# Kernel optimization log

Hardware: AMD Instinct MI355X
Metric: run time of the kernel (lower is better)

## Reference

```python
import jax, jax.numpy as jnp
import numpy as np

N, M = 100000, 12
A, E = 128, 64
BN_EPS = 1e-5

def batchnorm(x, gamma, beta):
    # training-mode BN over leading dim, biased variance (torch default)
    mean = jnp.mean(x, axis=0)
    var = jnp.var(x, axis=0)
    return (x - mean) * jax.lax.rsqrt(var + BN_EPS) * gamma + beta

def setup_inputs() -> dict:
    key = jax.random.key(0)
    ks = jax.random.split(key, 9)
    s_in = 1.0 / np.sqrt(2 * A + E)
    s_skip = 1.0 / np.sqrt(A)
    return {
        "atom_in_fea": jax.random.normal(ks[0], (N, A), jnp.float32),
        "nbr_fea": jax.random.normal(ks[1], (N, M, E), jnp.float32),
        "nbr_fea_idx": jax.random.randint(ks[2], (N, M), 0, N),
        "W_full": jax.random.uniform(ks[3], (2 * A + E, 2 * A), jnp.float32, -s_in, s_in),
        "b_full": jax.random.uniform(ks[4], (2 * A,), jnp.float32, -s_in, s_in),
        "gamma1": jnp.ones((2 * A,), jnp.float32),
        "beta1": jnp.zeros((2 * A,), jnp.float32),
        "gamma2": jnp.ones((A,), jnp.float32),
        "beta2": jnp.zeros((A,), jnp.float32),
        "W_skip": jax.random.uniform(ks[5], (A, A), jnp.float32, -s_skip, s_skip),
        "b_skip": jax.random.uniform(ks[6], (A,), jnp.float32, -s_skip, s_skip),
    }

def reference(atom_in_fea, nbr_fea, nbr_fea_idx, W_full, b_full,
              gamma1, beta1, gamma2, beta2, W_skip, b_skip):
    atom_nbr_fea = atom_in_fea[nbr_fea_idx]                      # [N,M,A] gather
    atom_self_fea = jnp.broadcast_to(atom_in_fea[:, None, :], (N, M, A))
    total = jnp.concatenate([atom_self_fea, atom_nbr_fea, nbr_fea], axis=2)  # [N,M,2A+E]
    gated = jnp.einsum('nmf,fg->nmg', total, W_full) + b_full    # [N,M,2A]
    gated = batchnorm(gated.reshape(-1, 2 * A), gamma1, beta1).reshape(N, M, 2 * A)
    nbr_filter, nbr_core = gated[..., :A], gated[..., A:]
    nbr_sumed = jnp.sum(jax.nn.sigmoid(nbr_filter) * jax.nn.softplus(nbr_core), axis=1)  # [N,A]
    nbr_sumed = batchnorm(nbr_sumed, gamma2, beta2)
    skip_val = atom_in_fea @ W_skip + b_skip
    return jax.nn.softplus(skip_val + nbr_sumed)
```

## Files before the change

kernel.cpp:

```cpp
#include <hip/hip_runtime.h>
#include <stdint.h>

#define N_ATOM 100000
#define M_NBR 12
#define A_FEA 128
#define E_FEA 64
#define KDIM 320
#define GDIM 256
#define ROWS (N_ATOM*M_NBR)
#define BN_EPS 1e-5f

typedef unsigned short u16;
typedef unsigned int u32;
typedef __attribute__((ext_vector_type(8))) short short8;
typedef __attribute__((ext_vector_type(4))) float f32x4;

#define S_BN1SUM 0
#define S_BN1SSQ 256
#define S_S1 512
#define S_T1 768
#define S_BN2SUM 1024
#define S_BN2SSQ 1152
#define S_S2 1280
#define S_T2 1408
#define STATS_F32 1536

#define WPQ_OFF 0
#define W3_OFF 131072
#define WSK_OFF 163840
#define STATS_OFF 196608
#define P_OFF 202752
#define PQ_BYTES ((size_t)N_ATOM*256*2)
#define Q_OFF (P_OFF + PQ_BYTES)
#define GATED_OFF (Q_OFF + PQ_BYTES)
#define GATED_BYTES ((size_t)ROWS*256*2)

__device__ __forceinline__ u16 f2bf(float x) {
    union { float f; u32 u; } v; v.f = x;
    u32 r = v.u + 0x7FFFu + ((v.u >> 16) & 1u);
    return (u16)(r >> 16);
}
__device__ __forceinline__ float bf2f(u16 u) {
    union { u32 u; float f; } v; v.u = ((u32)u) << 16;
    return v.f;
}
__device__ __forceinline__ float softplus_f(float x) {
    return fmaxf(x, 0.f) + __logf(1.f + __expf(-fabsf(x)));
}
__device__ __forceinline__ float sigmoid_f(float x) {
    return 1.f / (1.f + __expf(-x));
}

__global__ void zero_stats(float* __restrict__ stats) {
    int t = threadIdx.x;
    stats[t] = 0.f;
    stats[256 + t] = 0.f;
    stats[1024 + t] = 0.f;
}

__global__ void finalize1(const float* __restrict__ g1, const float* __restrict__ b1,
                          float* __restrict__ stats) {
    int c = threadIdx.x;
    const float inv_cnt = 1.f / (float)ROWS;
    float mean = stats[S_BN1SUM + c] * inv_cnt;
    float var  = stats[S_BN1SSQ + c] * inv_cnt - mean * mean;
    float iv = rsqrtf(var + BN_EPS);
    float s = g1[c] * iv;
    stats[S_S1 + c] = s;
    stats[S_T1 + c] = fmaf(-mean, s, b1[c]);
}

__global__ void finalize2(const float* __restrict__ g2, const float* __restrict__ b2,
                          float* __restrict__ stats) {
    int c = threadIdx.x;
    const float inv_cnt = 1.f / (float)N_ATOM;
    float mean = stats[S_BN2SUM + c] * inv_cnt;
    float var  = stats[S_BN2SSQ + c] * inv_cnt - mean * mean;
    float iv = rsqrtf(var + BN_EPS);
    float s = g2[c] * iv;
    stats[S_S2 + c] = s;
    stats[S_T2 + c] = fmaf(-mean, s, b2[c]);
}


__global__ void prep_pack_fast(const float* __restrict__ Wfull,
                               const float* __restrict__ Wskip,
                               u16* __restrict__ wpq, u16* __restrict__ w3,
                               u16* __restrict__ wsk) {
    int tid = blockIdx.x * blockDim.x + threadIdx.x;
    int l = tid & 63, fr = l & 15, fq = l >> 4;
    if (tid < 8192) {
        int ct = (tid >> 6) & 31;
        int kt = tid >> 11;
        int c = ct * 16 + fr;
        int k0 = kt * 32 + fq * 8;
        u16 tmp[8];
        #pragma unroll
        for (int i = 0; i < 8; ++i) {
            int kk = k0 + i;
            float v = (c < 256) ? Wfull[kk * GDIM + c]
                                : Wfull[(128 + kk) * GDIM + (c - 256)];
            tmp[i] = f2bf(v);
        }
        uint4 pk;
        pk.x = (u32)tmp[0] | ((u32)tmp[1] << 16);
        pk.y = (u32)tmp[2] | ((u32)tmp[3] << 16);
        pk.z = (u32)tmp[4] | ((u32)tmp[5] << 16);
        pk.w = (u32)tmp[6] | ((u32)tmp[7] << 16);
        *reinterpret_cast<uint4*>(&wpq[tid * 8]) = pk;
    } else if (tid < 10240) {
        int t2 = tid - 8192;
        int ct = (t2 >> 6) & 15;
        int kt = t2 >> 10;
        int c = ct * 16 + fr;
        int k0 = kt * 32 + fq * 8;
        u16 tmp[8];
        #pragma unroll
        for (int i = 0; i < 8; ++i) tmp[i] = f2bf(Wfull[(256 + k0 + i) * GDIM + c]);
        uint4 pk;
        pk.x = (u32)tmp[0] | ((u32)tmp[1] << 16);
        pk.y = (u32)tmp[2] | ((u32)tmp[3] << 16);
        pk.z = (u32)tmp[4] | ((u32)tmp[5] << 16);
        pk.w = (u32)tmp[6] | ((u32)tmp[7] << 16);
        *reinterpret_cast<uint4*>(&w3[t2 * 8]) = pk;
    } else if (tid < 12288) {
        int t3 = tid - 10240;
        int ct = (t3 >> 6) & 7;
        int kt = t3 >> 9;
        int c = ct * 16 + fr;
        int k0 = kt * 32 + fq * 8;
        u16 tmp[8];
        #pragma unroll
        for (int i = 0; i < 8; ++i) tmp[i] = f2bf(Wskip[(k0 + i) * A_FEA + c]);
        uint4 pk;
        pk.x = (u32)tmp[0] | ((u32)tmp[1] << 16);
        pk.y = (u32)tmp[2] | ((u32)tmp[3] << 16);
        pk.z = (u32)tmp[4] | ((u32)tmp[5] << 16);
        pk.w = (u32)tmp[6] | ((u32)tmp[7] << 16);
        *reinterpret_cast<uint4*>(&wsk[t3 * 8]) = pk;
    }
}

__launch_bounds__(256)
__global__ void pq_kernel(const float* __restrict__ atom_in,
                          const u16* __restrict__ wpq,
                          u16* __restrict__ Pb, u16* __restrict__ Qb) {
    __shared__ u16 al[64 * 130];
    const int t = threadIdx.x;
    const int w = t >> 6, l = t & 63, fr = l & 15, fq = l >> 4;
    const int n0 = blockIdx.x * 64;

    #pragma unroll
    for (int it = 0; it < 4; ++it) {
        int c = t + it * 256;
        int row = c >> 4, seg = c & 15;
        int n = n0 + row;
        uint4 pk = {0u, 0u, 0u, 0u};
        if (n < N_ATOM) {
            const float* src = atom_in + (size_t)n * A_FEA + seg * 8;
            float4 x0 = *reinterpret_cast<const float4*>(src);
            float4 x1 = *reinterpret_cast<const float4*>(src + 4);
            pk.x = (u32)f2bf(x0.x) | ((u32)f2bf(x0.y) << 16);
            pk.y = (u32)f2bf(x0.z) | ((u32)f2bf(x0.w) << 16);
            pk.z = (u32)f2bf(x1.x) | ((u32)f2bf(x1.y) << 16);
            pk.w = (u32)f2bf(x1.z) | ((u32)f2bf(x1.w) << 16);
        }
        *reinterpret_cast<uint4*>(&al[row * 130 + seg * 8]) = pk;
    }
    __syncthreads();

    f32x4 acc[4][8];
    #pragma unroll
    for (int rt = 0; rt < 4; ++rt)
        #pragma unroll
        for (int p = 0; p < 8; ++p)
            acc[rt][p] = (f32x4){0.f,0.f,0.f,0.f};

    for (int kt = 0; kt < 4; ++kt) {
        short8 af[4], bf[8];
        #pragma unroll
        for (int rt = 0; rt < 4; ++rt)
            af[rt] = *reinterpret_cast<const short8*>(
                &al[(rt * 16 + fr) * 130 + kt * 32 + fq * 8]);
        #pragma unroll
        for (int p = 0; p < 8; ++p)
            bf[p] = *reinterpret_cast<const short8*>(
                &wpq[((kt * 32 + w * 8 + p) * 64 + l) * 8]);
        #pragma unroll
        for (int rt = 0; rt < 4; ++rt)
            #pragma unroll
            for (int p = 0; p < 8; ++p)
                acc[rt][p] = __builtin_amdgcn_mfma_f32_16x16x32_bf16(
                    af[rt], bf[p], acc[rt][p], 0, 0, 0);
    }

    #pragma unroll
    for (int p = 0; p < 8; ++p) {
        int col = w * 128 + p * 16 + fr;
        u16* dst = (col < 256) ? Pb : Qb;
        int cc = (col < 256) ? col : (col - 256);
        #pragma unroll
        for (int rt = 0; rt < 4; ++rt)
            #pragma unroll
            for (int j = 0; j < 4; ++j) {
                int n = n0 + rt * 16 + fq * 4 + j;
                if (n < N_ATOM) dst[(size_t)n * 256 + cc] = f2bf(acc[rt][p][j]);
            }
    }
}

#define NTILES_E (ROWS/96)
#define GRID_E 2500
template<int MODE, int WG>
__launch_bounds__(512)
__global__ void estage_kernel(const float* __restrict__ nbr_fea,
                              const int* __restrict__ nbr_idx,
                              const u16* __restrict__ w3,
                              const u16* __restrict__ Pb,
                              const u16* __restrict__ Qb,
                              float* __restrict__ stats,
                              u16* __restrict__ gated,
                              float* __restrict__ out_ns) {
    constexpr int SH_BYTES = (MODE == 1) ? (96 * 66 * 2) : (96 * 132 * 4);
    __shared__ __align__(16) unsigned char shraw[SH_BYTES];
    u16* e_lds = (u16*)shraw;
    float* act = (float*)shraw;
    __shared__ int idx_lds[96];

    const int t = threadIdx.x;
    const int w = t >> 6, l = t & 63, fr = l & 15, fq = l >> 4;

    const int col0 = w * 16 + fr;
    const int col1 = 128 + col0;

    float s1v0, t1v0, s1v1, t1v1;
    if (MODE == 2) {
        s1v0 = stats[S_S1 + col0]; t1v0 = stats[S_T1 + col0];
        s1v1 = stats[S_S1 + col1]; t1v1 = stats[S_T1 + col1];
    }
    float ls0 = 0.f, lq0 = 0.f, ls1 = 0.f, lq1 = 0.f;
    float bsum = 0.f, bssq = 0.f;

    for (int tile = blockIdx.x; tile < NTILES_E; tile += GRID_E) {
        const int r0 = tile * 96;

        __syncthreads();
        for (int c = t; c < 768; c += 512) {
            int row = c >> 3, seg = c & 7;
            const float* src = nbr_fea + (size_t)(r0 + row) * E_FEA + seg * 8;
            float4 x0 = *reinterpret_cast<const float4*>(src);
            float4 x1 = *reinterpret_cast<const float4*>(src + 4);
            uint4 pk;
            pk.x = (u32)f2bf(x0.x) | ((u32)f2bf(x0.y) << 16);
            pk.y = (u32)f2bf(x0.z) | ((u32)f2bf(x0.w) << 16);
            pk.z = (u32)f2bf(x1.x) | ((u32)f2bf(x1.y) << 16);
            pk.w = (u32)f2bf(x1.z) | ((u32)f2bf(x1.w) << 16);
            *reinterpret_cast<uint4*>(&e_lds[row * 66 + seg * 8]) = pk;
        }
        if (t < 96) idx_lds[t] = nbr_idx[r0 + t];
        __syncthreads();

        f32x4 acc[6][2];
        #pragma unroll
        for (int rt = 0; rt < 6; ++rt) {
            acc[rt][0] = (f32x4){0.f,0.f,0.f,0.f};
            acc[rt][1] = (f32x4){0.f,0.f,0.f,0.f};
        }
        #pragma unroll
        for (int kt = 0; kt < 2; ++kt) {
            short8 af[6], bf0, bf1;
            #pragma unroll
            for (int rt = 0; rt < 6; ++rt)
                af[rt] = *reinterpret_cast<const short8*>(
                    &e_lds[(rt * 16 + fr) * 66 + kt * 32 + fq * 8]);
            bf0 = *reinterpret_cast<const short8*>(&w3[((kt * 16 + w) * 64 + l) * 8]);
            bf1 = *reinterpret_cast<const short8*>(&w3[((kt * 16 + 8 + w) * 64 + l) * 8]);
            #pragma unroll
            for (int rt = 0; rt < 6; ++rt) {
                acc[rt][0] = __builtin_amdgcn_mfma_f32_16x16x32_bf16(af[rt], bf0, acc[rt][0], 0, 0, 0);
                acc[rt][1] = __builtin_amdgcn_mfma_f32_16x16x32_bf16(af[rt], bf1, acc[rt][1], 0, 0, 0);
            }
        }

        if (MODE == 2) __syncthreads();

        #pragma unroll
        for (int rt = 0; rt < 6; ++rt) {
            #pragma unroll
            for (int j = 0; j < 4; ++j) {
                int row = rt * 16 + fq * 4 + j;
                int ag = tile * 8 + row / 12;
                int jr = idx_lds[row];
                const u16* prow = Pb + (size_t)ag * 256;
                const u16* qrow = Qb + (size_t)jr * 256;
                float g0 = acc[rt][0][j] + bf2f(prow[col0]) + bf2f(qrow[col0]);
                float g1 = acc[rt][1][j] + bf2f(prow[col1]) + bf2f(qrow[col1]);
                if (MODE == 1) {
                    ls0 += g0; lq0 = fmaf(g0, g0, lq0);
                    ls1 += g1; lq1 = fmaf(g1, g1, lq1);
                    if (WG) {
                        gated[(size_t)(r0 + row) * 256 + col0] = f2bf(g0);
                        gated[(size_t)(r0 + row) * 256 + col1] = f2bf(g1);
                    }
                } else {
                    float gf = fmaf(g0, s1v0, t1v0);
                    float gc = fmaf(g1, s1v1, t1v1);
                    act[row * 132 + col0] = sigmoid_f(gf) * softplus_f(gc);
                }
            }
        }

        if (MODE == 2) {
            __syncthreads();
            #pragma unroll
            for (int i = 0; i < 2; ++i) {
                int o = i * 512 + t;
                int a = o >> 7;
                int c = o & 127;
                float S = 0.f;
                #pragma unroll
                for (int mm = 0; mm < 12; ++mm)
                    S += act[(a * 12 + mm) * 132 + c];
                out_ns[(size_t)(tile * 8 + a) * A_FEA + c] = S;
                bsum += S;
                bssq = fmaf(S, S, bssq);
            }
        }
    }

    if (MODE == 1) {
        float s, q;
        s = ls0 + __shfl_xor(ls0, 16, 64); s += __shfl_xor(s, 32, 64);
        q = lq0 + __shfl_xor(lq0, 16, 64); q += __shfl_xor(q, 32, 64);
        if (fq == 0) {
            atomicAdd(&stats[S_BN1SUM + col0], s);
            atomicAdd(&stats[S_BN1SSQ + col0], q);
        }
        s = ls1 + __shfl_xor(ls1, 16, 64); s += __shfl_xor(s, 32, 64);
        q = lq1 + __shfl_xor(lq1, 16, 64); q += __shfl_xor(q, 32, 64);
        if (fq == 0) {
            atomicAdd(&stats[S_BN1SUM + col1], s);
            atomicAdd(&stats[S_BN1SSQ + col1], q);
        }
    } else {
        __syncthreads();
        if (t >= 128) {
            act[(t - 128) * 2]     = bsum;
            act[(t - 128) * 2 + 1] = bssq;
        }
        __syncthreads();
        if (t < 128) {
            bsum += act[t * 2]       + act[(128 + t) * 2]       + act[(256 + t) * 2];
            bssq += act[t * 2 + 1]   + act[(128 + t) * 2 + 1]   + act[(256 + t) * 2 + 1];
            atomicAdd(&stats[S_BN2SUM + t], bsum);
            atomicAdd(&stats[S_BN2SSQ + t], bssq);
        }
    }
}

__launch_bounds__(256)
__global__ void apply_kernel(const u16* __restrict__ gated,
                             float* __restrict__ stats,
                             float* __restrict__ out) {
    __shared__ float red[4][64][4];
    const int t = threadIdx.x;
    const int lidc = t & 63, aoff = t >> 6;
    const int c0 = lidc * 2;
    const int n0 = blockIdx.x * 64;

    const float s1f0 = stats[S_S1 + c0],     t1f0 = stats[S_T1 + c0];
    const float s1f1 = stats[S_S1 + c0 + 1], t1f1 = stats[S_T1 + c0 + 1];
    const float s1c0 = stats[S_S1 + 128 + c0],     t1c0 = stats[S_T1 + 128 + c0];
    const float s1c1 = stats[S_S1 + 128 + c0 + 1], t1c1 = stats[S_T1 + 128 + c0 + 1];

    float bs0 = 0.f, bq0 = 0.f, bs1 = 0.f, bq1 = 0.f;

    for (int a = aoff; a < 64; a += 4) {
        int n = n0 + a;
        if (n >= N_ATOM) continue;
        float S0 = 0.f, S1 = 0.f;
        const u16* base = gated + (size_t)n * 12 * 256;
        #pragma unroll
        for (int m = 0; m < 12; ++m) {
            u32 uf = *reinterpret_cast<const u32*>(base + m * 256 + c0);
            u32 uc = *reinterpret_cast<const u32*>(base + m * 256 + 128 + c0);
            float f0 = __uint_as_float(uf << 16);
            float f1 = __uint_as_float(uf & 0xFFFF0000u);
            float c_0 = __uint_as_float(uc << 16);
            float c_1 = __uint_as_float(uc & 0xFFFF0000u);
            float gf0 = fmaf(f0, s1f0, t1f0), gf1 = fmaf(f1, s1f1, t1f1);
            float gc0 = fmaf(c_0, s1c0, t1c0), gc1 = fmaf(c_1, s1c1, t1c1);
            S0 += sigmoid_f(gf0) * softplus_f(gc0);
            S1 += sigmoid_f(gf1) * softplus_f(gc1);
        }
        *reinterpret_cast<float2*>(&out[(size_t)n * A_FEA + c0]) = make_float2(S0, S1);
        bs0 += S0; bq0 = fmaf(S0, S0, bq0);
        bs1 += S1; bq1 = fmaf(S1, S1, bq1);
    }

    red[aoff][lidc][0] = bs0; red[aoff][lidc][1] = bq0;
    red[aoff][lidc][2] = bs1; red[aoff][lidc][3] = bq1;
    __syncthreads();
    if (t < 64) {
        float a0 = red[0][t][0] + red[1][t][0] + red[2][t][0] + red[3][t][0];
        float a1 = red[0][t][1] + red[1][t][1] + red[2][t][1] + red[3][t][1];
        float a2 = red[0][t][2] + red[1][t][2] + red[2][t][2] + red[3][t][2];
        float a3 = red[0][t][3] + red[1][t][3] + red[2][t][3] + red[3][t][3];
        atomicAdd(&stats[S_BN2SUM + 2 * t],     a0);
        atomicAdd(&stats[S_BN2SSQ + 2 * t],     a1);
        atomicAdd(&stats[S_BN2SUM + 2 * t + 1], a2);
        atomicAdd(&stats[S_BN2SSQ + 2 * t + 1], a3);
    }
}

#define BM5 64
__launch_bounds__(256, 2)
__global__ void skip_kernel(const float* __restrict__ atom_in,
                            const u16* __restrict__ wsf,
                            const float* __restrict__ b_skip,
                            const float* __restrict__ stats,
                            float* __restrict__ out) {
    __shared__ u16 a5[BM5 * 136];
    const int t = threadIdx.x;
    const int w = t >> 6, l = t & 63, fr = l & 15, fq = l >> 4;
    const int n0 = blockIdx.x * BM5;

    #pragma unroll
    for (int it = 0; it < 4; ++it) {
        int c = t + it * 256;
        int row = c >> 4, seg = c & 15;
        int n = n0 + row;
        uint4 pk = {0u, 0u, 0u, 0u};
        if (n < N_ATOM) {
            const float* src = atom_in + (size_t)n * A_FEA + seg * 8;
            float4 x0 = *reinterpret_cast<const float4*>(src);
            float4 x1 = *reinterpret_cast<const float4*>(src + 4);
            pk.x = (u32)f2bf(x0.x) | ((u32)f2bf(x0.y) << 16);
            pk.y = (u32)f2bf(x0.z) | ((u32)f2bf(x0.w) << 16);
            pk.z = (u32)f2bf(x1.x) | ((u32)f2bf(x1.y) << 16);
            pk.w = (u32)f2bf(x1.z) | ((u32)f2bf(x1.w) << 16);
        }
        *reinterpret_cast<uint4*>(&a5[row * 136 + seg * 8]) = pk;
    }
    __syncthreads();

    f32x4 acc[4][2];
    #pragma unroll
    for (int rt = 0; rt < 4; ++rt) {
        acc[rt][0] = (f32x4){0.f,0.f,0.f,0.f};
        acc[rt][1] = (f32x4){0.f,0.f,0.f,0.f};
    }
    for (int kt = 0; kt < 4; ++kt) {
        short8 af[4], bf[2];
        #pragma unroll
        for (int rt = 0; rt < 4; ++rt)
            af[rt] = *reinterpret_cast<const short8*>(
                &a5[(rt * 16 + fr) * 136 + kt * 32 + fq * 8]);
        #pragma unroll
        for (int p = 0; p < 2; ++p)
            bf[p] = *reinterpret_cast<const short8*>(
                &wsf[((kt * 8 + 2 * w + p) * 64 + l) * 8]);
        #pragma unroll
        for (int rt = 0; rt < 4; ++rt)
            #pragma unroll
            for (int p = 0; p < 2; ++p)
                acc[rt][p] = __builtin_amdgcn_mfma_f32_16x16x32_bf16(
                    af[rt], bf[p], acc[rt][p], 0, 0, 0);
    }

    #pragma unroll
    for (int p = 0; p < 2; ++p) {
        int col = w * 32 + p * 16 + fr;
        float bs = b_skip[col];
        float s2 = stats[S_S2 + col];
        float t2 = stats[S_T2 + col];
        #pragma unroll
        for (int rt = 0; rt < 4; ++rt)
            #pragma unroll
            for (int j = 0; j < 4; ++j) {
                int n = n0 + rt * 16 + fq * 4 + j;
                if (n < N_ATOM) {
                    size_t o = (size_t)n * A_FEA + col;
                    float S = out[o];
                    out[o] = softplus_f(acc[rt][p][j] + bs + fmaf(S, s2, t2));
                }
            }
    }
}

#define BM 96
#define NTILES (ROWS/BM)
#define GRID_P 2500
#define TPB 256
#define APAD 328
#define ACTPAD 132

__global__ void prep_pack_slow(const float* __restrict__ Wfull,
                               const float* __restrict__ Wskip,
                               u16* __restrict__ wf, u16* __restrict__ wsf) {
    int tid = blockIdx.x * blockDim.x + threadIdx.x;
    if (tid < 10240) {
        int l = tid & 63;
        int ct = (tid >> 6) & 15;
        int kt = tid >> 10;
        int fr = l & 15, fq = l >> 4;
        int col = ct * 16 + fr;
        int k0 = kt * 32 + fq * 8;
        u16 tmp[8];
        #pragma unroll
        for (int i = 0; i < 8; ++i) tmp[i] = f2bf(Wfull[(k0 + i) * GDIM + col]);
        uint4 pk;
        pk.x = (u32)tmp[0] | ((u32)tmp[1] << 16);
        pk.y = (u32)tmp[2] | ((u32)tmp[3] << 16);
        pk.z = (u32)tmp[4] | ((u32)tmp[5] << 16);
        pk.w = (u32)tmp[6] | ((u32)tmp[7] << 16);
        *reinterpret_cast<uint4*>(&wf[tid * 8]) = pk;
    } else if (tid < 12288) {
        int t2 = tid - 10240;
        int l = t2 & 63;
        int ct = (t2 >> 6) & 7;
        int kt = t2 >> 9;
        int fr = l & 15, fq = l >> 4;
        int col = ct * 16 + fr;
        int k0 = kt * 32 + fq * 8;
        u16 tmp[8];
        #pragma unroll
        for (int i = 0; i < 8; ++i) tmp[i] = f2bf(Wskip[(k0 + i) * A_FEA + col]);
        uint4 pk;
        pk.x = (u32)tmp[0] | ((u32)tmp[1] << 16);
        pk.y = (u32)tmp[2] | ((u32)tmp[3] << 16);
        pk.z = (u32)tmp[4] | ((u32)tmp[5] << 16);
        pk.w = (u32)tmp[6] | ((u32)tmp[7] << 16);
        *reinterpret_cast<uint4*>(&wsf[t2 * 8]) = pk;
    }
}

template<int PASS>
__launch_bounds__(TPB, 2)
__global__ void pass_kernel(const float* __restrict__ atom_in,
                            const float* __restrict__ nbr_fea,
                            const int* __restrict__ nbr_idx,
                            const u16* __restrict__ wf,
                            float* __restrict__ stats,
                            float* __restrict__ out_ns) {
    __shared__ union {
        u16 a[BM * APAD];
        float act[BM * ACTPAD];
    } sh;

    const int t = threadIdx.x;
    const int w = t >> 6, l = t & 63, fr = l & 15, fq = l >> 4;
    const int ct0 = 2 * w;

    int colp[4];
    colp[0] = ct0 * 16 + fr;
    colp[1] = colp[0] + 16;
    colp[2] = colp[0] + 128;
    colp[3] = colp[1] + 128;

    float s1v[4], t1v[4];
    if (PASS == 2) {
        #pragma unroll
        for (int p = 0; p < 4; ++p) {
            s1v[p] = stats[S_S1 + colp[p]];
            t1v[p] = stats[S_T1 + colp[p]];
        }
    }
    float ls[4] = {0.f,0.f,0.f,0.f}, lq[4] = {0.f,0.f,0.f,0.f};
    float bsum = 0.f, bssq = 0.f;

    for (int tile = blockIdx.x; tile < NTILES; tile += GRID_P) {
        const int n0 = tile * 8;

        __syncthreads();
        for (int it = 0; it < 15; ++it) {
            int c = t + it * TPB;
            int row = c / 40;
            int seg = c - row * 40;
            int an = row / 12;
            int m  = row - an * 12;
            int na = n0 + an;
            const float* src;
            if (seg < 16) {
                src = atom_in + (size_t)na * A_FEA + seg * 8;
            } else if (seg < 32) {
                int j = nbr_idx[na * M_NBR + m];
                src = atom_in + (size_t)j * A_FEA + (seg - 16) * 8;
            } else {
                src = nbr_fea + ((size_t)na * M_NBR + m) * E_FEA + (seg - 32) * 8;
            }
            float4 x0 = *reinterpret_cast<const float4*>(src);
            float4 x1 = *reinterpret_cast<const float4*>(src + 4);
            uint4 pk;
            pk.x = (u32)f2bf(x0.x) | ((u32)f2bf(x0.y) << 16);
            pk.y = (u32)f2bf(x0.z) | ((u32)f2bf(x0.w) << 16);
            pk.z = (u32)f2bf(x1.x) | ((u32)f2bf(x1.y) << 16);
            pk.w = (u32)f2bf(x1.z) | ((u32)f2bf(x1.w) << 16);
            *reinterpret_cast<uint4*>(&sh.a[row * APAD + seg * 8]) = pk;
        }
        __syncthreads();

        f32x4 acc[6][4];
        #pragma unroll
        for (int rt = 0; rt < 6; ++rt)
            #pragma unroll
            for (int p = 0; p < 4; ++p)
                acc[rt][p] = (f32x4){0.f,0.f,0.f,0.f};

        for (int kt = 0; kt < 10; ++kt) {
            short8 af[6], bf[4];
            #pragma unroll
            for (int rt = 0; rt < 6; ++rt)
                af[rt] = *reinterpret_cast<const short8*>(
                    &sh.a[(rt * 16 + fr) * APAD + kt * 32 + fq * 8]);
            #pragma unroll
            for (int p = 0; p < 4; ++p) {
                int ct = (p < 2) ? (ct0 + p) : (ct0 + 8 + (p - 2));
                bf[p] = *reinterpret_cast<const short8*>(
                    &wf[((kt * 16 + ct) * 64 + l) * 8]);
            }
            #pragma unroll
            for (int rt = 0; rt < 6; ++rt)
                #pragma unroll
                for (int p = 0; p < 4; ++p)
                    acc[rt][p] = __builtin_amdgcn_mfma_f32_16x16x32_bf16(
                        af[rt], bf[p], acc[rt][p], 0, 0, 0);
        }

        if (PASS == 1) {
            #pragma unroll
            for (int p = 0; p < 4; ++p)
                #pragma unroll
                for (int rt = 0; rt < 6; ++rt)
                    #pragma unroll
                    for (int j = 0; j < 4; ++j) {
                        float v = acc[rt][p][j];
                        ls[p] += v;
                        lq[p] = fmaf(v, v, lq[p]);
                    }
        } else {
            __syncthreads();
            #pragma unroll
            for (int rt = 0; rt < 6; ++rt)
                #pragma unroll
                for (int p = 0; p < 2; ++p)
                    #pragma unroll
                    for (int j = 0; j < 4; ++j) {
                        float gf = fmaf(acc[rt][p][j],     s1v[p],     t1v[p]);
                        float gc = fmaf(acc[rt][2 + p][j], s1v[2 + p], t1v[2 + p]);
                        float a = sigmoid_f(gf) * softplus_f(gc);
                        int row = rt * 16 + fq * 4 + j;
                        int colact = ct0 * 16 + p * 16 + fr;
                        sh.act[row * ACTPAD + colact] = a;
                    }
            __syncthreads();
            #pragma unroll
            for (int i = 0; i < 4; ++i) {
                int o = i * TPB + t;
                int a = o >> 7;
                int c = o & 127;
                float S = 0.f;
                #pragma unroll
                for (int mm = 0; mm < 12; ++mm)
                    S += sh.act[(a * 12 + mm) * ACTPAD + c];
                out_ns[(size_t)(n0 + a) * A_FEA + c] = S;
                bsum += S;
                bssq = fmaf(S, S, bssq);
            }
        }
    }

    if (PASS == 1) {
        #pragma unroll
        for (int p = 0; p < 4; ++p) {
            float s = ls[p], q = lq[p];
            s += __shfl_xor(s, 16, 64);
            s += __shfl_xor(s, 32, 64);
            q += __shfl_xor(q, 16, 64);
            q += __shfl_xor(q, 32, 64);
            if (fq == 0) {
                atomicAdd(&stats[S_BN1SUM + colp[p]], s);
                atomicAdd(&stats[S_BN1SSQ + colp[p]], q);
            }
        }
    } else {
        __syncthreads();
        if (t >= 128) {
            sh.act[(t - 128) * 2]     = bsum;
            sh.act[(t - 128) * 2 + 1] = bssq;
        }
        __syncthreads();
        if (t < 128) {
            bsum += sh.act[t * 2];
            bssq += sh.act[t * 2 + 1];
            atomicAdd(&stats[S_BN2SUM + t], bsum);
            atomicAdd(&stats[S_BN2SSQ + t], bssq);
        }
    }
}

extern "C" void kernel_launch(void* const* d_in, const int* in_sizes, int n_in,
                              void* d_out, int out_size, void* d_ws, size_t ws_size,
                              hipStream_t stream) {
    (void)in_sizes; (void)n_in; (void)out_size;
    const float* atom_in = (const float*)d_in[0];
    const float* nbr_fea = (const float*)d_in[1];
    const int*   nbr_idx = (const int*)d_in[2];
    const float* Wfull   = (const float*)d_in[3];
    const float* g1      = (const float*)d_in[5];
    const float* b1      = (const float*)d_in[6];
    const float* g2      = (const float*)d_in[7];
    const float* b2      = (const float*)d_in[8];
    const float* Wsk     = (const float*)d_in[9];
    const float* bsk     = (const float*)d_in[10];
    float* out = (float*)d_out;

    float* stats = (float*)((char*)d_ws + STATS_OFF);
    u16* wskf = (u16*)((char*)d_ws + WSK_OFF);

    const size_t need_mid  = GATED_OFF;
    const size_t need_fast = GATED_OFF + GATED_BYTES;

    if (ws_size >= need_mid) {
        u16* wpq = (u16*)d_ws;
        u16* w3  = (u16*)((char*)d_ws + W3_OFF);
        u16* Pb  = (u16*)((char*)d_ws + P_OFF);
        u16* Qb  = (u16*)((char*)d_ws + Q_OFF);
        u16* gated = (u16*)((char*)d_ws + GATED_OFF);

        zero_stats<<<1, 256, 0, stream>>>(stats);
        prep_pack_fast<<<48, 256, 0, stream>>>(Wfull, Wsk, wpq, w3, wskf);
        pq_kernel<<<(N_ATOM + 63) / 64, 256, 0, stream>>>(atom_in, wpq, Pb, Qb);
        if (ws_size >= need_fast) {
            estage_kernel<1, 1><<<GRID_E, 512, 0, stream>>>(
                nbr_fea, nbr_idx, w3, Pb, Qb, stats, gated, out);
            finalize1<<<1, 256, 0, stream>>>(g1, b1, stats);
            apply_kernel<<<(N_ATOM + 63) / 64, 256, 0, stream>>>(gated, stats, out);
        } else {
            estage_kernel<1, 0><<<GRID_E, 512, 0, stream>>>(
                nbr_fea, nbr_idx, w3, Pb, Qb, stats, (u16*)d_ws, out);
            finalize1<<<1, 256, 0, stream>>>(g1, b1, stats);
            estage_kernel<2, 0><<<GRID_E, 512, 0, stream>>>(
                nbr_fea, nbr_idx, w3, Pb, Qb, stats, (u16*)d_ws, out);
        }
        finalize2<<<1, 128, 0, stream>>>(g2, b2, stats);
        skip_kernel<<<(N_ATOM + BM5 - 1) / BM5, 256, 0, stream>>>(atom_in, wskf, bsk, stats, out);
    } else {
        u16* wf = (u16*)d_ws;
        zero_stats<<<1, 256, 0, stream>>>(stats);
        prep_pack_slow<<<48, 256, 0, stream>>>(Wfull, Wsk, wf, wskf);
        pass_kernel<1><<<GRID_P, TPB, 0, stream>>>(atom_in, nbr_fea, nbr_idx, wf, stats, out);
        finalize1<<<1, 256, 0, stream>>>(g1, b1, stats);
        pass_kernel<2><<<GRID_P, TPB, 0, stream>>>(atom_in, nbr_fea, nbr_idx, wf, stats, out);
        finalize2<<<1, 128, 0, stream>>>(g2, b2, stats);
        skip_kernel<<<(N_ATOM + BM5 - 1) / BM5, 256, 0, stream>>>(atom_in, wskf, bsk, stats, out);
    }
}
```

Measured before the change: 812.8 us.

## Drop materialized gated buffer; recompute in second pass with LDS-staged P/Q rows

Removes the bf16 gated intermediate and its apply kernel, and always runs two recomputing passes of the edge-stage GEMM (stats pass, then apply pass). P rows and the gathered Q rows for each tile are now staged into LDS with coalesced vector loads, replacing per-element scattered global reads in the epilogue. This trades writing and re-reading a large gated buffer for re-reading nbr_fea and redoing the small MFMA GEMM, and it raises LDS use per block.

```diff
diff --git a/kernel.cpp b/kernel.cpp
--- a/kernel.cpp
+++ b/kernel.cpp
@@ -32,8 +32,7 @@
 #define P_OFF 202752
 #define PQ_BYTES ((size_t)N_ATOM*256*2)
 #define Q_OFF (P_OFF + PQ_BYTES)
-#define GATED_OFF (Q_OFF + PQ_BYTES)
-#define GATED_BYTES ((size_t)ROWS*256*2)
+#define NEED_MID (Q_OFF + PQ_BYTES)
 
 __device__ __forceinline__ u16 f2bf(float x) {
     union { float f; u32 u; } v; v.f = x;
@@ -81,7 +80,6 @@
     stats[S_S2 + c] = s;
     stats[S_T2 + c] = fmaf(-mean, s, b2[c]);
 }
-
 
 __global__ void prep_pack_fast(const float* __restrict__ Wfull,
                                const float* __restrict__ Wskip,
@@ -211,29 +209,36 @@
 
 #define NTILES_E (ROWS/96)
 #define GRID_E 2500
-template<int MODE, int WG>
-__launch_bounds__(512)
-__global__ void estage_kernel(const float* __restrict__ nbr_fea,
-                              const int* __restrict__ nbr_idx,
-                              const u16* __restrict__ w3,
-                              const u16* __restrict__ Pb,
-                              const u16* __restrict__ Qb,
-                              float* __restrict__ stats,
-                              u16* __restrict__ gated,
-                              float* __restrict__ out_ns) {
-    constexpr int SH_BYTES = (MODE == 1) ? (96 * 66 * 2) : (96 * 132 * 4);
-    __shared__ __align__(16) unsigned char shraw[SH_BYTES];
+#define EPAD 66
+#define PPAD 264
+#define QPAD 268
+#define ACTPAD2 134
+#define P_SH (96*EPAD*2)
+#define Q_SH (P_SH + 8*PPAD*2)
+#define SH_TOTAL (Q_SH + 96*QPAD*2)
+
+template<int MODE>
+__launch_bounds__(512, 4)
+__global__ void estage2(const float* __restrict__ nbr_fea,
+                        const int* __restrict__ nbr_idx,
+                        const u16* __restrict__ w3,
+                        const u16* __restrict__ Pb,
+                        const u16* __restrict__ Qb,
+                        float* __restrict__ stats,
+                        float* __restrict__ out_ns) {
+    __shared__ __align__(16) unsigned char shraw[SH_TOTAL];
     u16* e_lds = (u16*)shraw;
-    float* act = (float*)shraw;
-    __shared__ int idx_lds[96];
+    u16* p_lds = (u16*)(shraw + P_SH);
+    u16* q_lds = (u16*)(shraw + Q_SH);
+    float* act = (float*)(shraw + Q_SH);
+    float* red = (float*)shraw;
 
     const int t = threadIdx.x;
     const int w = t >> 6, l = t & 63, fr = l & 15, fq = l >> 4;
-
     const int col0 = w * 16 + fr;
     const int col1 = 128 + col0;
 
-    float s1v0, t1v0, s1v1, t1v1;
+    float s1v0 = 0.f, t1v0 = 0.f, s1v1 = 0.f, t1v1 = 0.f;
     if (MODE == 2) {
         s1v0 = stats[S_S1 + col0]; t1v0 = stats[S_T1 + col0];
         s1v1 = stats[S_S1 + col1]; t1v1 = stats[S_T1 + col1];
@@ -243,21 +248,38 @@
 
     for (int tile = blockIdx.x; tile < NTILES_E; tile += GRID_E) {
         const int r0 = tile * 96;
+        const int n0a = tile * 8;
 
         __syncthreads();
-        for (int c = t; c < 768; c += 512) {
-            int row = c >> 3, seg = c & 7;
-            const float* src = nbr_fea + (size_t)(r0 + row) * E_FEA + seg * 8;
-            float4 x0 = *reinterpret_cast<const float4*>(src);
-            float4 x1 = *reinterpret_cast<const float4*>(src + 4);
-            uint4 pk;
-            pk.x = (u32)f2bf(x0.x) | ((u32)f2bf(x0.y) << 16);
-            pk.y = (u32)f2bf(x0.z) | ((u32)f2bf(x0.w) << 16);
-            pk.z = (u32)f2bf(x1.x) | ((u32)f2bf(x1.y) << 16);
-            pk.w = (u32)f2bf(x1.z) | ((u32)f2bf(x1.w) << 16);
-            *reinterpret_cast<uint4*>(&e_lds[row * 66 + seg * 8]) = pk;
-        }
-        if (t < 96) idx_lds[t] = nbr_idx[r0 + t];
+
+        #pragma unroll
+        for (int i = 0; i < 2; ++i) {
+            int o = t + i * 512;
+            if (o < 768) {
+                int row = o >> 3, seg = o & 7;
+                const float* src = nbr_fea + (size_t)(r0 + row) * E_FEA + seg * 8;
+                float4 x0 = *reinterpret_cast<const float4*>(src);
+                float4 x1 = *reinterpret_cast<const float4*>(src + 4);
+                uint4 pk;
+                pk.x = (u32)f2bf(x0.x) | ((u32)f2bf(x0.y) << 16);
+                pk.y = (u32)f2bf(x0.z) | ((u32)f2bf(x0.w) << 16);
+                pk.z = (u32)f2bf(x1.x) | ((u32)f2bf(x1.y) << 16);
+                pk.w = (u32)f2bf(x1.z) | ((u32)f2bf(x1.w) << 16);
+                *reinterpret_cast<uint4*>(&e_lds[row * EPAD + seg * 8]) = pk;
+            }
+        }
+        if (t < 256) {
+            int row = t >> 5, seg = t & 31;
+            *reinterpret_cast<uint4*>(&p_lds[row * PPAD + seg * 8]) =
+                *reinterpret_cast<const uint4*>(&Pb[(size_t)(n0a + row) * 256 + seg * 8]);
+        }
+        #pragma unroll
+        for (int i = 0; i < 12; ++i) {
+            int row = i * 8 + w;
+            int jr = nbr_idx[r0 + row];
+            *reinterpret_cast<uint2*>(&q_lds[row * QPAD + l * 4]) =
+                *reinterpret_cast<const uint2*>(&Qb[(size_t)jr * 256 + l * 4]);
+        }
         __syncthreads();
 
         f32x4 acc[6][2];
@@ -272,7 +294,7 @@
             #pragma unroll
             for (int rt = 0; rt < 6; ++rt)
                 af[rt] = *reinterpret_cast<const short8*>(
-                    &e_lds[(rt * 16 + fr) * 66 + kt * 32 + fq * 8]);
+                    &e_lds[(rt * 16 + fr) * EPAD + kt * 32 + fq * 8]);
             bf0 = *reinterpret_cast<const short8*>(&w3[((kt * 16 + w) * 64 + l) * 8]);
             bf1 = *reinterpret_cast<const short8*>(&w3[((kt * 16 + 8 + w) * 64 + l) * 8]);
             #pragma unroll
@@ -282,46 +304,55 @@
             }
         }
 
-        if (MODE == 2) __syncthreads();
-
-        #pragma unroll
-        for (int rt = 0; rt < 6; ++rt) {
-            #pragma unroll
-            for (int j = 0; j < 4; ++j) {
-                int row = rt * 16 + fq * 4 + j;
-                int ag = tile * 8 + row / 12;
-                int jr = idx_lds[row];
-                const u16* prow = Pb + (size_t)ag * 256;
-                const u16* qrow = Qb + (size_t)jr * 256;
-                float g0 = acc[rt][0][j] + bf2f(prow[col0]) + bf2f(qrow[col0]);
-                float g1 = acc[rt][1][j] + bf2f(prow[col1]) + bf2f(qrow[col1]);
-                if (MODE == 1) {
+        if (MODE == 1) {
+            #pragma unroll
+            for (int rt = 0; rt < 6; ++rt)
+                #pragma unroll
+                for (int j = 0; j < 4; ++j) {
+                    int row = rt * 16 + fq * 4 + j;
+                    int atom = (row * 171) >> 11;
+                    float g0 = acc[rt][0][j] + bf2f(p_lds[atom * PPAD + col0])
+                                             + bf2f(q_lds[row * QPAD + col0]);
+                    float g1 = acc[rt][1][j] + bf2f(p_lds[atom * PPAD + col1])
+                                             + bf2f(q_lds[row * QPAD + col1]);
                     ls0 += g0; lq0 = fmaf(g0, g0, lq0);
                     ls1 += g1; lq1 = fmaf(g1, g1, lq1);
-                    if (WG) {
-                        gated[(size_t)(r0 + row) * 256 + col0] = f2bf(g0);
-                        gated[(size_t)(r0 + row) * 256 + col1] = f2bf(g1);
-                    }
-                } else {
+                }
+        } else {
+            float ar[24];
+            #pragma unroll
+            for (int rt = 0; rt < 6; ++rt)
+                #pragma unroll
+                for (int j = 0; j < 4; ++j) {
+                    int row = rt * 16 + fq * 4 + j;
+                    int atom = (row * 171) >> 11;
+                    float g0 = acc[rt][0][j] + bf2f(p_lds[atom * PPAD + col0])
+                                             + bf2f(q_lds[row * QPAD + col0]);
+                    float g1 = acc[rt][1][j] + bf2f(p_lds[atom * PPAD + col1])
+                                             + bf2f(q_lds[row * QPAD + col1]);
                     float gf = fmaf(g0, s1v0, t1v0);
                     float gc = fmaf(g1, s1v1, t1v1);
-                    act[row * 132 + col0] = sigmoid_f(gf) * softplus_f(gc);
+                    ar[rt * 4 + j] = sigmoid_f(gf) * softplus_f(gc);
                 }
-            }
-        }
-
-        if (MODE == 2) {
+            __syncthreads();
+            #pragma unroll
+            for (int rt = 0; rt < 6; ++rt)
+                #pragma unroll
+                for (int j = 0; j < 4; ++j) {
+                    int row = rt * 16 + fq * 4 + j;
+                    act[row * ACTPAD2 + col0] = ar[rt * 4 + j];
+                }
             __syncthreads();
             #pragma unroll
             for (int i = 0; i < 2; ++i) {
                 int o = i * 512 + t;
                 int a = o >> 7;
-                int c = o & 127;
+                int c = t & 127;
                 float S = 0.f;
                 #pragma unroll
                 for (int mm = 0; mm < 12; ++mm)
-                    S += act[(a * 12 + mm) * 132 + c];
-                out_ns[(size_t)(tile * 8 + a) * A_FEA + c] = S;
+                    S += act[(a * 12 + mm) * ACTPAD2 + c];
+                out_ns[(size_t)(n0a + a) * A_FEA + c] = S;
                 bsum += S;
                 bssq = fmaf(S, S, bssq);
             }
@@ -345,71 +376,16 @@
     } else {
         __syncthreads();
         if (t >= 128) {
-            act[(t - 128) * 2]     = bsum;
-            act[(t - 128) * 2 + 1] = bssq;
+            red[(t - 128) * 2]     = bsum;
+            red[(t - 128) * 2 + 1] = bssq;
         }
         __syncthreads();
         if (t < 128) {
-            bsum += act[t * 2]       + act[(128 + t) * 2]       + act[(256 + t) * 2];
-            bssq += act[t * 2 + 1]   + act[(128 + t) * 2 + 1]   + act[(256 + t) * 2 + 1];
+            bsum += red[t * 2]     + red[(128 + t) * 2]     + red[(256 + t) * 2];
+            bssq += red[t * 2 + 1] + red[(128 + t) * 2 + 1] + red[(256 + t) * 2 + 1];
             atomicAdd(&stats[S_BN2SUM + t], bsum);
             atomicAdd(&stats[S_BN2SSQ + t], bssq);
         }
-    }
-}
-
-__launch_bounds__(256)
-__global__ void apply_kernel(const u16* __restrict__ gated,
-                             float* __restrict__ stats,
-                             float* __restrict__ out) {
-    __shared__ float red[4][64][4];
-    const int t = threadIdx.x;
-    const int lidc = t & 63, aoff = t >> 6;
-    const int c0 = lidc * 2;
-    const int n0 = blockIdx.x * 64;
-
-    const float s1f0 = stats[S_S1 + c0],     t1f0 = stats[S_T1 + c0];
-    const float s1f1 = stats[S_S1 + c0 + 1], t1f1 = stats[S_T1 + c0 + 1];
-    const float s1c0 = stats[S_S1 + 128 + c0],     t1c0 = stats[S_T1 + 128 + c0];
-    const float s1c1 = stats[S_S1 + 128 + c0 + 1], t1c1 = stats[S_T1 + 128 + c0 + 1];
-
-    float bs0 = 0.f, bq0 = 0.f, bs1 = 0.f, bq1 = 0.f;
-
-    for (int a = aoff; a < 64; a += 4) {
-        int n = n0 + a;
-        if (n >= N_ATOM) continue;
-        float S0 = 0.f, S1 = 0.f;
-        const u16* base = gated + (size_t)n * 12 * 256;
-        #pragma unroll
-        for (int m = 0; m < 12; ++m) {
-            u32 uf = *reinterpret_cast<const u32*>(base + m * 256 + c0);
-            u32 uc = *reinterpret_cast<const u32*>(base + m * 256 + 128 + c0);
-            float f0 = __uint_as_float(uf << 16);
-            float f1 = __uint_as_float(uf & 0xFFFF0000u);
-            float c_0 = __uint_as_float(uc << 16);
-            float c_1 = __uint_as_float(uc & 0xFFFF0000u);
-            float gf0 = fmaf(f0, s1f0, t1f0), gf1 = fmaf(f1, s1f1, t1f1);
-            float gc0 = fmaf(c_0, s1c0, t1c0), gc1 = fmaf(c_1, s1c1, t1c1);
-            S0 += sigmoid_f(gf0) * softplus_f(gc0);
-            S1 += sigmoid_f(gf1) * softplus_f(gc1);
-        }
-        *reinterpret_cast<float2*>(&out[(size_t)n * A_FEA + c0]) = make_float2(S0, S1);
-        bs0 += S0; bq0 = fmaf(S0, S0, bq0);
-        bs1 += S1; bq1 = fmaf(S1, S1, bq1);
-    }
-
-    red[aoff][lidc][0] = bs0; red[aoff][lidc][1] = bq0;
-    red[aoff][lidc][2] = bs1; red[aoff][lidc][3] = bq1;
-    __syncthreads();
-    if (t < 64) {
-        float a0 = red[0][t][0] + red[1][t][0] + red[2][t][0] + red[3][t][0];
-        float a1 = red[0][t][1] + red[1][t][1] + red[2][t][1] + red[3][t][1];
-        float a2 = red[0][t][2] + red[1][t][2] + red[2][t][2] + red[3][t][2];
-        float a3 = red[0][t][3] + red[1][t][3] + red[2][t][3] + red[3][t][3];
-        atomicAdd(&stats[S_BN2SUM + 2 * t],     a0);
-        atomicAdd(&stats[S_BN2SSQ + 2 * t],     a1);
-        atomicAdd(&stats[S_BN2SUM + 2 * t + 1], a2);
-        atomicAdd(&stats[S_BN2SSQ + 2 * t + 1], a3);
     }
 }
 
@@ -718,31 +694,18 @@
     float* stats = (float*)((char*)d_ws + STATS_OFF);
     u16* wskf = (u16*)((char*)d_ws + WSK_OFF);
 
-    const size_t need_mid  = GATED_OFF;
-    const size_t need_fast = GATED_OFF + GATED_BYTES;
-
-    if (ws_size >= need_mid) {
+    if (ws_size >= NEED_MID) {
         u16* wpq = (u16*)d_ws;
         u16* w3  = (u16*)((char*)d_ws + W3_OFF);
         u16* Pb  = (u16*)((char*)d_ws + P_OFF);
         u16* Qb  = (u16*)((char*)d_ws + Q_OFF);
-        u16* gated = (u16*)((char*)d_ws + GATED_OFF);
 
         zero_stats<<<1, 256, 0, stream>>>(stats);
         prep_pack_fast<<<48, 256, 0, stream>>>(Wfull, Wsk, wpq, w3, wskf);
         pq_kernel<<<(N_ATOM + 63) / 64, 256, 0, stream>>>(atom_in, wpq, Pb, Qb);
-        if (ws_size >= need_fast) {
-            estage_kernel<1, 1><<<GRID_E, 512, 0, stream>>>(
-                nbr_fea, nbr_idx, w3, Pb, Qb, stats, gated, out);
-            finalize1<<<1, 256, 0, stream>>>(g1, b1, stats);
-            apply_kernel<<<(N_ATOM + 63) / 64, 256, 0, stream>>>(gated, stats, out);
-        } else {
-            estage_kernel<1, 0><<<GRID_E, 512, 0, stream>>>(
-                nbr_fea, nbr_idx, w3, Pb, Qb, stats, (u16*)d_ws, out);
-            finalize1<<<1, 256, 0, stream>>>(g1, b1, stats);
-            estage_kernel<2, 0><<<GRID_E, 512, 0, stream>>>(
-                nbr_fea, nbr_idx, w3, Pb, Qb, stats, (u16*)d_ws, out);
-        }
+        estage2<1><<<GRID_E, 512, 0, stream>>>(nbr_fea, nbr_idx, w3, Pb, Qb, stats, out);
+        finalize1<<<1, 256, 0, stream>>>(g1, b1, stats);
+        estage2<2><<<GRID_E, 512, 0, stream>>>(nbr_fea, nbr_idx, w3, Pb, Qb, stats, out);
         finalize2<<<1, 128, 0, stream>>>(g2, b2, stats);
         skip_kernel<<<(N_ATOM + BM5 - 1) / BM5, 256, 0, stream>>>(atom_in, wskf, bsk, stats, out);
     } else {
```

New measurement: 853.6 us. 5.0% more time.
